# Optimization experiments

Hardware: AMD Instinct MI355X
Metric: run time of the kernel (lower is better)

Reference implementation:

```python
import jax, jax.numpy as jnp
import numpy as np

DIM = 192
HEADS = 6
WS = 8          # window size
SHIFT = 4       # shift size
HIDDEN = 384    # mlp hidden = 2.0 * dim
EPS = 1e-5


def _rel_pos_index(ws):
    # static [N, N] int index into the (2*ws-1)^2 bias table
    coords = np.stack(np.meshgrid(np.arange(ws), np.arange(ws), indexing='ij')).reshape(2, -1)
    rel = (coords[:, :, None] - coords[:, None, :]).transpose(1, 2, 0)
    rel[..., 0] += ws - 1
    rel[..., 1] += ws - 1
    rel[..., 0] *= 2 * ws - 1
    return rel.sum(-1)


def _attn_mask(hp, wp, ws, shift):
    # static shift-window mask: [nW, N, N], 0 or -100
    img = np.zeros((hp, wp))
    sl = (slice(0, -ws), slice(-ws, -shift), slice(-shift, None))
    cnt = 0
    for hs in sl:
        for wsl in sl:
            img[hs, wsl] = cnt
            cnt += 1
    m = img.reshape(hp // ws, ws, wp // ws, ws).transpose(0, 2, 1, 3).reshape(-1, ws * ws)
    diff = m[:, None, :] - m[:, :, None]
    return np.where(diff != 0, -100.0, 0.0).astype(np.float32)


def _ln(x, g, b):
    mu = x.mean(-1, keepdims=True)
    var = ((x - mu) ** 2).mean(-1, keepdims=True)
    return (x - mu) * jax.lax.rsqrt(var + EPS) * g + b


def setup_inputs() -> dict:
    key = jax.random.key(0)
    ks = jax.random.split(key, 6)
    B, H, W, C = 4, 224, 224, DIM
    return {
        'x': jax.random.normal(ks[0], (B, H * W, C), jnp.float32),
        'norm1_g': jnp.ones((C,), jnp.float32),
        'norm1_b': jnp.zeros((C,), jnp.float32),
        'qkv_w': jax.random.normal(ks[1], (C, 3 * C), jnp.float32) * 0.02,
        'qkv_b': jnp.zeros((3 * C,), jnp.float32),
        'proj_w': jax.random.normal(ks[2], (C, C), jnp.float32) * 0.02,
        'proj_b': jnp.zeros((C,), jnp.float32),
        'rel_bias_table': jax.random.normal(ks[3], ((2 * WS - 1) ** 2, HEADS), jnp.float32) * 0.02,
        'norm2_g': jnp.ones((C,), jnp.float32),
        'norm2_b': jnp.zeros((C,), jnp.float32),
        'fc1_w': jax.random.normal(ks[4], (C, HIDDEN), jnp.float32) * 0.02,
        'fc1_b': jnp.zeros((HIDDEN,), jnp.float32),
        'fc2_w': jax.random.normal(ks[5], (HIDDEN, C), jnp.float32) * 0.02,
        'fc2_b': jnp.zeros((C,), jnp.float32),
        'height': 224,
        'width': 224,
    }


def reference(x, norm1_g, norm1_b, qkv_w, qkv_b, proj_w, proj_b, rel_bias_table,
              norm2_g, norm2_b, fc1_w, fc1_b, fc2_w, fc2_b, height, width):
    B, T, C = x.shape
    dh = C // HEADS
    scale = dh ** (-0.5)
    shortcut = x

    xw = _ln(x, norm1_g, norm1_b).reshape(B, height, width, C)
    pad_h = (WS - height % WS) % WS
    pad_w = (WS - width % WS) % WS
    if pad_h > 0 or pad_w > 0:
        xw = jnp.pad(xw, ((0, 0), (0, pad_h), (0, pad_w), (0, 0)))
    Hp, Wp = height + pad_h, width + pad_w

    if SHIFT > 0:
        xs = jnp.roll(xw, (-SHIFT, -SHIFT), axis=(1, 2))
        mask = jnp.asarray(_attn_mask(Hp, Wp, WS, SHIFT))  # [nW, N, N]
    else:
        xs, mask = xw, None

    N = WS * WS
    # window partition -> [B*nW, N, C]
    xwin = xs.reshape(B, Hp // WS, WS, Wp // WS, WS, C).transpose(0, 1, 3, 2, 4, 5).reshape(-1, N, C)

    qkv = (xwin @ qkv_w + qkv_b).reshape(-1, N, 3, HEADS, dh).transpose(2, 0, 3, 1, 4)
    q, k, v = qkv[0] * scale, qkv[1], qkv[2]          # [B*nW, H, N, dh]
    attn = jnp.einsum('whnd,whmd->whnm', q, k)         # [B*nW, H, N, N]

    idx = jnp.asarray(_rel_pos_index(WS).reshape(-1))
    bias = rel_bias_table[idx].reshape(N, N, HEADS).transpose(2, 0, 1)  # [H, N, N]
    attn = attn + bias[None]

    if mask is not None:
        nW = mask.shape[0]
        attn = attn.reshape(-1, nW, HEADS, N, N) + mask[None, :, None]
        attn = attn.reshape(-1, HEADS, N, N)

    attn = jax.nn.softmax(attn, axis=-1)
    out = jnp.einsum('whnm,whmd->wnhd', attn, v).reshape(-1, N, C)
    out = out @ proj_w + proj_b

    # window reverse -> [B, Hp, Wp, C]
    out = out.reshape(B, Hp // WS, Wp // WS, WS, WS, C).transpose(0, 1, 3, 2, 4, 5).reshape(B, Hp, Wp, C)
    if SHIFT > 0:
        out = jnp.roll(out, (SHIFT, SHIFT), axis=(1, 2))
    if pad_h > 0 or pad_w > 0:
        out = out[:, :height, :width, :]

    x = shortcut + out.reshape(B, height * width, C)
    h = _ln(x, norm2_g, norm2_b)
    h = jax.nn.gelu(h @ fc1_w + fc1_b, approximate=False) @ fc2_w + fc2_b
    return x + h
```

## Files before the change

kernel.cpp:

```cpp
#include <hip/hip_runtime.h>
#include <math.h>

#define T_TOT   200704
#define C_DIM   192
#define HEADS   6
#define DH      32
#define NTOK    64
#define NWIN    3136
#define HID     384
#define IMG     224
#define NSIDE   28
#define WPI     784
#define QSCALE  0.17677669529663687f

typedef unsigned short ushortT;
typedef short bf16x8 __attribute__((ext_vector_type(8)));
typedef float f32x4 __attribute__((ext_vector_type(4)));

__device__ __forceinline__ float bf_lo(unsigned u){ return __uint_as_float(u << 16); }
__device__ __forceinline__ float bf_hi(unsigned u){ return __uint_as_float(u & 0xFFFF0000u); }
__device__ __forceinline__ unsigned short f2bf(float f){
    unsigned u = __float_as_uint(f);
    u += 0x7FFFu + ((u >> 16) & 1u);
    return (unsigned short)(u >> 16);
}
__device__ __forceinline__ unsigned pack2(float a, float b){
    return (unsigned)f2bf(a) | ((unsigned)f2bf(b) << 16);
}

__global__ void k_wprep(const float* __restrict__ w, unsigned short* __restrict__ o, int K, int N)
{
    int idx = blockIdx.x * 256 + threadIdx.x;
    if (idx >= K * N) return;
    int n = idx / K, k = idx - n * K;
    o[idx] = f2bf(w[(size_t)k * N + n]);
}

__global__ void k_bmprep(const float* __restrict__ table, float* __restrict__ bmT)
{
    int idx = blockIdx.x * 256 + threadIdx.x;
    int q = idx & 63, m = (idx >> 6) & 63;
    int head = (idx >> 12) % HEADS, type = idx / (64 * 64 * HEADS);
    int rq = q >> 3, cq = q & 7, rm = m >> 3, cm = m & 7;
    float b = table[((rq - rm + 7) * 15 + (cq - cm + 7)) * HEADS + head];
    int th = type >> 1, tw = type & 1;
    int lq = (th ? (rq >= 4 ? 2 : 1) : 0) * 3 + (tw ? (cq >= 4 ? 2 : 1) : 0);
    int lm = (th ? (rm >= 4 ? 2 : 1) : 0) * 3 + (tw ? (cm >= 4 ? 2 : 1) : 0);
    bmT[idx] = b + ((lq != lm) ? -100.f : 0.f);
}

__global__ void k_ln1qkv(const float* __restrict__ x, const float* __restrict__ g,
                         const float* __restrict__ bta,
                         const unsigned short* __restrict__ wt, const float* __restrict__ bias,
                         unsigned short* __restrict__ q, unsigned short* __restrict__ k,
                         unsigned short* __restrict__ v)
{
    __shared__ __align__(16) unsigned short As[64*200];
    const int tid = threadIdx.x, lane = tid & 63, wid = tid >> 6;
    const int lr = lane & 15, lg = lane >> 4;
    const int win = blockIdx.x;

    {
        int n = tid >> 2, part = tid & 3;
        int bimg = win / WPI, w2 = win % WPI;
        int wi = w2 / NSIDE, wj = w2 % NSIDE;
        int r = n >> 3, c = n & 7;
        int hs = wi * 8 + r + 4; if (hs >= IMG) hs -= IMG;
        int ws = wj * 8 + c + 4; if (ws >= IMG) ws -= IMG;
        size_t s = ((size_t)bimg * (IMG*IMG) + hs * IMG + ws) * C_DIM;
        const float* xp = x + s + part * 48;
        float vals[48];
        float sum = 0.f, sq = 0.f;
        #pragma unroll
        for (int j = 0; j < 12; j++){
            float4 v4 = *(const float4*)(xp + j*4);
            vals[j*4+0] = v4.x; vals[j*4+1] = v4.y; vals[j*4+2] = v4.z; vals[j*4+3] = v4.w;
            sum += v4.x + v4.y + v4.z + v4.w;
            sq  += v4.x*v4.x + v4.y*v4.y + v4.z*v4.z + v4.w*v4.w;
        }
        sum += __shfl_xor(sum, 1); sq += __shfl_xor(sq, 1);
        sum += __shfl_xor(sum, 2); sq += __shfl_xor(sq, 2);
        float mu = sum * (1.f/192.f);
        float var = sq * (1.f/192.f) - mu*mu;
        float rs = rsqrtf(var + 1e-5f);
        int c0 = part * 48;
        #pragma unroll
        for (int j = 0; j < 6; j++){
            int cc = c0 + j*8;
            float4 ga = *(const float4*)(g + cc), gb = *(const float4*)(g + cc + 4);
            float4 ba = *(const float4*)(bta + cc), bb = *(const float4*)(bta + cc + 4);
            unsigned short tmp[8];
            tmp[0] = f2bf((vals[j*8+0]-mu)*rs*ga.x + ba.x);
            tmp[1] = f2bf((vals[j*8+1]-mu)*rs*ga.y + ba.y);
            tmp[2] = f2bf((vals[j*8+2]-mu)*rs*ga.z + ba.z);
            tmp[3] = f2bf((vals[j*8+3]-mu)*rs*ga.w + ba.w);
            tmp[4] = f2bf((vals[j*8+4]-mu)*rs*gb.x + bb.x);
            tmp[5] = f2bf((vals[j*8+5]-mu)*rs*gb.y + bb.y);
            tmp[6] = f2bf((vals[j*8+6]-mu)*rs*gb.z + bb.z);
            tmp[7] = f2bf((vals[j*8+7]-mu)*rs*gb.w + bb.w);
            *(uint4*)&As[n*200 + cc] = *(uint4*)tmp;
        }
    }
    __syncthreads();

    #pragma unroll
    for (int chunk = 0; chunk < 3; chunk++){
        f32x4 acc[3][4];
        #pragma unroll
        for (int nf = 0; nf < 3; nf++)
            #pragma unroll
            for (int mf = 0; mf < 4; mf++)
                acc[nf][mf] = (f32x4){0.f,0.f,0.f,0.f};
        #pragma unroll
        for (int k0 = 0; k0 < C_DIM; k0 += 32){
            bf16x8 a[4], b[3];
            #pragma unroll
            for (int mf = 0; mf < 4; mf++)
                a[mf] = *(const bf16x8*)&As[(mf*16 + lr)*200 + k0 + lg*8];
            #pragma unroll
            for (int nf = 0; nf < 3; nf++)
                b[nf] = *(const bf16x8*)(wt + (size_t)(chunk*192 + wid*48 + nf*16 + lr)*C_DIM + k0 + lg*8);
            #pragma unroll
            for (int nf = 0; nf < 3; nf++)
                #pragma unroll
                for (int mf = 0; mf < 4; mf++)
                    acc[nf][mf] = __builtin_amdgcn_mfma_f32_16x16x32_bf16(a[mf], b[nf], acc[nf][mf], 0, 0, 0);
        }
        unsigned short* dst = (chunk == 0) ? q : (chunk == 1) ? k : v;
        float sc = (chunk == 0) ? QSCALE : 1.f;
        #pragma unroll
        for (int nf = 0; nf < 3; nf++){
            int cc = wid*48 + nf*16 + lr;
            float b = bias[chunk*192 + cc];
            int head = cc >> 5, d = cc & 31;
            unsigned short* dp = dst + ((size_t)(win*HEADS + head) * NTOK) * DH + d;
            #pragma unroll
            for (int mf = 0; mf < 4; mf++)
                #pragma unroll
                for (int r = 0; r < 4; r++){
                    int ntok = mf*16 + lg*4 + r;
                    dp[ntok*DH] = f2bf((acc[nf][mf][r] + b) * sc);
                }
        }
    }
}

__global__ void k_attn_mfma(const unsigned short* __restrict__ q, const unsigned short* __restrict__ k,
                            const unsigned short* __restrict__ v, const float* __restrict__ bmT,
                            unsigned short* __restrict__ attn_o)
{
    __shared__ __align__(16) unsigned short Vt[4][32*72];
    __shared__ __align__(16) unsigned short Ps[4][64*72];
    const int tid = threadIdx.x, lane = tid & 63, wid = tid >> 6;
    const int wh = blockIdx.x * 4 + wid;
    const int head = wh % HEADS, win = wh / HEADS;
    const int w2 = win % WPI;
    const int type = ((w2 / NSIDE) == 27 ? 2 : 0) + ((w2 % NSIDE) == 27 ? 1 : 0);
    const size_t base = (size_t)wh * (NTOK * DH);
    const int lr = lane & 15, lg = lane >> 4;

    {
        const uint4* vp = (const uint4*)(v + base + lane * DH);
        uint4 va = vp[0], vb = vp[1], vc = vp[2], vd = vp[3];
        unsigned short* dst = &Vt[wid][lane];
        unsigned w0[8] = {va.x, va.y, va.z, va.w, vb.x, vb.y, vb.z, vb.w};
        #pragma unroll
        for (int j = 0; j < 8; j++){
            dst[(2*j)*72]   = (unsigned short)(w0[j] & 0xFFFFu);
            dst[(2*j+1)*72] = (unsigned short)(w0[j] >> 16);
        }
        unsigned w1[8] = {vc.x, vc.y, vc.z, vc.w, vd.x, vd.y, vd.z, vd.w};
        #pragma unroll
        for (int j = 0; j < 8; j++){
            dst[(16+2*j)*72]   = (unsigned short)(w1[j] & 0xFFFFu);
            dst[(16+2*j+1)*72] = (unsigned short)(w1[j] >> 16);
        }
    }

    bf16x8 aq[4], bk[4];
    {
        const unsigned short* qg = q + base + lr * DH + (lg << 3);
        const unsigned short* kg = k + base + lr * DH + (lg << 3);
        #pragma unroll
        for (int i = 0; i < 4; i++){
            aq[i] = *(const bf16x8*)(qg + i * 16 * DH);
            bk[i] = *(const bf16x8*)(kg + i * 16 * DH);
        }
    }

    f32x4 acc[4][4];
    #pragma unroll
    for (int mi = 0; mi < 4; mi++)
        #pragma unroll
        for (int ni = 0; ni < 4; ni++)
            acc[mi][ni] = __builtin_amdgcn_mfma_f32_16x16x32_bf16(aq[mi], bk[ni],
                              (f32x4){0.f,0.f,0.f,0.f}, 0, 0, 0);

    const float* bmBase = bmT + ((size_t)(type * HEADS + head) * 64) * 64;
    #pragma unroll
    for (int mi = 0; mi < 4; mi++)
        #pragma unroll
        for (int ni = 0; ni < 4; ni++){
            float4 bm = *(const float4*)(bmBase + (lr + 16*ni)*64 + lg*4 + 16*mi);
            acc[mi][ni][0] += bm.x; acc[mi][ni][1] += bm.y;
            acc[mi][ni][2] += bm.z; acc[mi][ni][3] += bm.w;
        }

    #pragma unroll
    for (int mi = 0; mi < 4; mi++){
        #pragma unroll
        for (int r = 0; r < 4; r++){
            float mx = fmaxf(fmaxf(acc[mi][0][r], acc[mi][1][r]),
                             fmaxf(acc[mi][2][r], acc[mi][3][r]));
            mx = fmaxf(mx, __shfl_xor(mx, 1));
            mx = fmaxf(mx, __shfl_xor(mx, 2));
            mx = fmaxf(mx, __shfl_xor(mx, 4));
            mx = fmaxf(mx, __shfl_xor(mx, 8));
            float e0 = __expf(acc[mi][0][r] - mx);
            float e1 = __expf(acc[mi][1][r] - mx);
            float e2 = __expf(acc[mi][2][r] - mx);
            float e3 = __expf(acc[mi][3][r] - mx);
            float sum = e0 + e1 + e2 + e3;
            sum += __shfl_xor(sum, 1);
            sum += __shfl_xor(sum, 2);
            sum += __shfl_xor(sum, 4);
            sum += __shfl_xor(sum, 8);
            float inv = 1.f / sum;
            int row = lg*4 + r + 16*mi;
            unsigned short* pr = &Ps[wid][row*72 + lr];
            pr[0]  = f2bf(e0 * inv);
            pr[16] = f2bf(e1 * inv);
            pr[32] = f2bf(e2 * inv);
            pr[48] = f2bf(e3 * inv);
        }
    }

    f32x4 o[4][2];
    #pragma unroll
    for (int mi = 0; mi < 4; mi++)
        #pragma unroll
        for (int ni = 0; ni < 2; ni++)
            o[mi][ni] = (f32x4){0.f,0.f,0.f,0.f};
    #pragma unroll
    for (int kb = 0; kb < 2; kb++){
        bf16x8 ap[4], bv[2];
        #pragma unroll
        for (int mi = 0; mi < 4; mi++)
            ap[mi] = *(const bf16x8*)&Ps[wid][(lr + 16*mi)*72 + (lg<<3) + 32*kb];
        #pragma unroll
        for (int ni = 0; ni < 2; ni++)
            bv[ni] = *(const bf16x8*)&Vt[wid][(lr + 16*ni)*72 + (lg<<3) + 32*kb];
        #pragma unroll
        for (int mi = 0; mi < 4; mi++)
            #pragma unroll
            for (int ni = 0; ni < 2; ni++)
                o[mi][ni] = __builtin_amdgcn_mfma_f32_16x16x32_bf16(ap[mi], bv[ni], o[mi][ni], 0, 0, 0);
    }

    unsigned short* ob = attn_o + ((size_t)win * NTOK) * C_DIM + head * DH;
    #pragma unroll
    for (int mi = 0; mi < 4; mi++)
        #pragma unroll
        for (int ni = 0; ni < 2; ni++)
            #pragma unroll
            for (int r = 0; r < 4; r++){
                int row = lg*4 + r + 16*mi;
                ob[(size_t)row * C_DIM + lr + 16*ni] = f2bf(o[mi][ni][r]);
            }
}

template<int KTOT>
__device__ __forceinline__ void mfma_tile(const unsigned short* __restrict__ A,
                                          const unsigned short* __restrict__ Wt,
                                          int t0, int n0,
                                          f32x4 acc[4][2],
                                          unsigned short* As, unsigned short* Bs)
{
    const int tid = threadIdx.x;
    const int lane = tid & 63, wid = tid >> 6;
    const int wm = wid >> 1, wn = wid & 1;
    const int lr = lane & 15, lk = (lane >> 4) << 3;
    #pragma unroll
    for (int i = 0; i < 4; i++)
        #pragma unroll
        for (int j = 0; j < 2; j++)
            acc[i][j] = (f32x4){0.f, 0.f, 0.f, 0.f};

    const int arow = tid >> 1, asoff = (tid & 1) << 4;

    for (int k0 = 0; k0 < KTOT; k0 += 32){
        __syncthreads();
        {
            const unsigned short* ga = A + (size_t)(t0 + arow)*KTOT + k0 + asoff;
            *(uint4*)&As[arow*40 + asoff]     = *(const uint4*)(ga);
            *(uint4*)&As[arow*40 + asoff + 8] = *(const uint4*)(ga + 8);
            if (tid < 128){
                const unsigned short* gb = Wt + (size_t)(n0 + arow)*KTOT + k0 + asoff;
                *(uint4*)&Bs[arow*40 + asoff]     = *(const uint4*)(gb);
                *(uint4*)&Bs[arow*40 + asoff + 8] = *(const uint4*)(gb + 8);
            }
        }
        __syncthreads();
        bf16x8 b0 = *(const bf16x8*)&Bs[(wn*32 +      lr)*40 + lk];
        bf16x8 b1 = *(const bf16x8*)&Bs[(wn*32 + 16 + lr)*40 + lk];
        #pragma unroll
        for (int mf = 0; mf < 4; mf++){
            bf16x8 a = *(const bf16x8*)&As[(wm*64 + mf*16 + lr)*40 + lk];
            acc[mf][0] = __builtin_amdgcn_mfma_f32_16x16x32_bf16(a, b0, acc[mf][0], 0, 0, 0);
            acc[mf][1] = __builtin_amdgcn_mfma_f32_16x16x32_bf16(a, b1, acc[mf][1], 0, 0, 0);
        }
    }
}

__global__ void k_proj_m(const unsigned short* __restrict__ ain, const unsigned short* __restrict__ wt,
                         const float* __restrict__ bias, const float* __restrict__ x,
                         float* __restrict__ out)
{
    __shared__ __align__(16) unsigned short As[128*40];
    __shared__ __align__(16) unsigned short Bs[64*40];
    int t0 = blockIdx.x * 128, n0 = blockIdx.y * 64;
    f32x4 acc[4][2];
    mfma_tile<C_DIM>(ain, wt, t0, n0, acc, As, Bs);

    const int tid = threadIdx.x, lane = tid & 63, wid = tid >> 6;
    const int wm = wid >> 1, wn = wid & 1, lr = lane & 15;
    float b0 = bias[n0 + wn*32 + lr];
    float b1 = bias[n0 + wn*32 + 16 + lr];
    #pragma unroll
    for (int mf = 0; mf < 4; mf++){
        #pragma unroll
        for (int r = 0; r < 4; r++){
            int t = t0 + wm*64 + mf*16 + ((lane >> 4) << 2) + r;
            int win = t >> 6, n = t & 63;
            int bimg = win / WPI, w2 = win % WPI;
            int wi = w2 / NSIDE, wj = w2 % NSIDE;
            int rr = n >> 3, cc = n & 7;
            int hf = wi*8 + rr + 4; if (hf >= IMG) hf -= IMG;
            int wf = wj*8 + cc + 4; if (wf >= IMG) wf -= IMG;
            size_t s = ((size_t)bimg*(IMG*IMG) + hf*IMG + wf) * C_DIM;
            int c0 = n0 + wn*32 + lr;
            out[s + c0]      = x[s + c0]      + acc[mf][0][r] + b0;
            out[s + c0 + 16] = x[s + c0 + 16] + acc[mf][1][r] + b1;
        }
    }
}

#define XS_STR 200
#define H1_STR 392
#define O_STR  196
__global__ void k_mlp(float* __restrict__ out,
                      const float* __restrict__ g, const float* __restrict__ bta,
                      const unsigned short* __restrict__ w1, const float* __restrict__ b1,
                      const unsigned short* __restrict__ w2, const float* __restrict__ b2)
{
    __shared__ __align__(16) unsigned short H1u[32*H1_STR];
    unsigned short* Xs = H1u;
    float* O = (float*)H1u;
    const int tid = threadIdx.x, lane = tid & 63, wid = tid >> 6;
    const int lr = lane & 15, lg = lane >> 4;
    const int t0 = blockIdx.x * 32;

    {
        int row = tid >> 3, part = tid & 7;
        const float* xp = out + (size_t)(t0 + row) * C_DIM + part * 24;
        float vals[24];
        float sum = 0.f, sq = 0.f;
        #pragma unroll
        for (int j = 0; j < 6; j++){
            float4 v4 = *(const float4*)(xp + j*4);
            vals[j*4+0] = v4.x; vals[j*4+1] = v4.y; vals[j*4+2] = v4.z; vals[j*4+3] = v4.w;
            sum += v4.x + v4.y + v4.z + v4.w;
            sq  += v4.x*v4.x + v4.y*v4.y + v4.z*v4.z + v4.w*v4.w;
        }
        sum += __shfl_xor(sum, 1); sq += __shfl_xor(sq, 1);
        sum += __shfl_xor(sum, 2); sq += __shfl_xor(sq, 2);
        sum += __shfl_xor(sum, 4); sq += __shfl_xor(sq, 4);
        float mu = sum * (1.f/192.f);
        float var = sq * (1.f/192.f) - mu*mu;
        float rs = rsqrtf(var + 1e-5f);
        int c0 = part * 24;
        #pragma unroll
        for (int j = 0; j < 3; j++){
            int c = c0 + j*8;
            float4 ga = *(const float4*)(g + c), gb = *(const float4*)(g + c + 4);
            float4 ba = *(const float4*)(bta + c), bb = *(const float4*)(bta + c + 4);
            unsigned short tmp[8];
            tmp[0] = f2bf((vals[j*8+0]-mu)*rs*ga.x + ba.x);
            tmp[1] = f2bf((vals[j*8+1]-mu)*rs*ga.y + ba.y);
            tmp[2] = f2bf((vals[j*8+2]-mu)*rs*ga.z + ba.z);
            tmp[3] = f2bf((vals[j*8+3]-mu)*rs*ga.w + ba.w);
            tmp[4] = f2bf((vals[j*8+4]-mu)*rs*gb.x + bb.x);
            tmp[5] = f2bf((vals[j*8+5]-mu)*rs*gb.y + bb.y);
            tmp[6] = f2bf((vals[j*8+6]-mu)*rs*gb.z + bb.z);
            tmp[7] = f2bf((vals[j*8+7]-mu)*rs*gb.w + bb.w);
            *(uint4*)&Xs[row*XS_STR + c] = *(uint4*)tmp;
        }
    }
    __syncthreads();

    f32x4 acc1[6][2];
    {
        #pragma unroll
        for (int mf = 0; mf < 6; mf++)
            #pragma unroll
            for (int nf = 0; nf < 2; nf++)
                acc1[mf][nf] = (f32x4){0.f,0.f,0.f,0.f};
        #pragma unroll
        for (int k0 = 0; k0 < C_DIM; k0 += 32){
            bf16x8 a[6], b[2];
            #pragma unroll
            for (int mf = 0; mf < 6; mf++)
                a[mf] = *(const bf16x8*)(w1 + (size_t)(wid*96 + mf*16 + lr)*C_DIM + k0 + lg*8);
            #pragma unroll
            for (int nf = 0; nf < 2; nf++)
                b[nf] = *(const bf16x8*)&Xs[(nf*16 + lr)*XS_STR + k0 + lg*8];
            #pragma unroll
            for (int mf = 0; mf < 6; mf++)
                #pragma unroll
                for (int nf = 0; nf < 2; nf++)
                    acc1[mf][nf] = __builtin_amdgcn_mfma_f32_16x16x32_bf16(a[mf], b[nf], acc1[mf][nf], 0, 0, 0);
        }
    }
    __syncthreads();

    {
        #pragma unroll
        for (int mf = 0; mf < 6; mf++){
            int hc = wid*96 + mf*16 + lg*4;
            float4 bb = *(const float4*)(b1 + hc);
            float bias[4] = {bb.x, bb.y, bb.z, bb.w};
            #pragma unroll
            for (int nf = 0; nf < 2; nf++){
                int token = nf*16 + lr;
                float gl[4];
                #pragma unroll
                for (int r = 0; r < 4; r++){
                    float u = acc1[mf][nf][r] + bias[r];
                    gl[r] = 0.5f*u*(1.f + erff(u*0.70710678118654752f));
                }
                uint2 pk; pk.x = pack2(gl[0], gl[1]); pk.y = pack2(gl[2], gl[3]);
                *(uint2*)&H1u[token*H1_STR + hc] = pk;
            }
        }
    }
    __syncthreads();

    f32x4 acc2[2][3];
    {
        #pragma unroll
        for (int rf = 0; rf < 2; rf++)
            #pragma unroll
            for (int cf = 0; cf < 3; cf++)
                acc2[rf][cf] = (f32x4){0.f,0.f,0.f,0.f};
        #pragma unroll
        for (int k0 = 0; k0 < HID; k0 += 32){
            bf16x8 a[2], b[3];
            #pragma unroll
            for (int rf = 0; rf < 2; rf++)
                a[rf] = *(const bf16x8*)&H1u[(rf*16 + lr)*H1_STR + k0 + lg*8];
            #pragma unroll
            for (int cf = 0; cf < 3; cf++)
                b[cf] = *(const bf16x8*)(w2 + (size_t)(wid*48 + cf*16 + lr)*HID + k0 + lg*8);
            #pragma unroll
            for (int rf = 0; rf < 2; rf++)
                #pragma unroll
                for (int cf = 0; cf < 3; cf++)
                    acc2[rf][cf] = __builtin_amdgcn_mfma_f32_16x16x32_bf16(a[rf], b[cf], acc2[rf][cf], 0, 0, 0);
        }
    }
    __syncthreads();

    #pragma unroll
    for (int cf = 0; cf < 3; cf++){
        int c = wid*48 + cf*16 + lr;
        float bias = b2[c];
        #pragma unroll
        for (int rf = 0; rf < 2; rf++)
            #pragma unroll
            for (int r = 0; r < 4; r++)
                O[(rf*16 + lg*4 + r)*O_STR + c] = acc2[rf][cf][r] + bias;
    }
    __syncthreads();

    {
        int row = tid >> 3, part = tid & 7;
        float* op = out + (size_t)(t0 + row) * C_DIM;
        const float* Or = O + row * O_STR;
        #pragma unroll
        for (int j = 0; j < 6; j++){
            int c = part*4 + j*32;
            float4 add = *(const float4*)&Or[c];
            float4 old = *(const float4*)&op[c];
            old.x += add.x; old.y += add.y; old.z += add.z; old.w += add.w;
            *(float4*)&op[c] = old;
        }
    }
}

extern "C" void kernel_launch(void* const* d_in, const int* in_sizes, int n_in,
                              void* d_out, int out_size, void* d_ws, size_t ws_size,
                              hipStream_t stream)
{
    const float* x       = (const float*)d_in[0];
    const float* n1g     = (const float*)d_in[1];
    const float* n1b     = (const float*)d_in[2];
    const float* qkv_w   = (const float*)d_in[3];
    const float* qkv_b   = (const float*)d_in[4];
    const float* proj_w  = (const float*)d_in[5];
    const float* proj_b  = (const float*)d_in[6];
    const float* rtab    = (const float*)d_in[7];
    const float* n2g     = (const float*)d_in[8];
    const float* n2b     = (const float*)d_in[9];
    const float* fc1_w   = (const float*)d_in[10];
    const float* fc1_b   = (const float*)d_in[11];
    const float* fc2_w   = (const float*)d_in[12];
    const float* fc2_b   = (const float*)d_in[13];
    float* out = (float*)d_out;

    char* wsb = (char*)d_ws;
    const size_t SZ = (size_t)T_TOT * C_DIM * 2;
    unsigned short* attn_o = (unsigned short*)(wsb);
    unsigned short* qb   = (unsigned short*)(wsb + SZ);
    unsigned short* kb   = (unsigned short*)(wsb + 2*SZ);
    unsigned short* vb   = (unsigned short*)(wsb + 3*SZ);
    unsigned short* wt_qkv  = (unsigned short*)(wsb + 4*SZ);
    unsigned short* wt_proj = wt_qkv + 576*192;
    unsigned short* wt_fc1  = wt_proj + 192*192;
    unsigned short* wt_fc2  = wt_fc1 + 384*192;
    float*          bmT     = (float*)(wt_fc2 + 384*192);

    k_wprep<<<(192*576 + 255)/256, 256, 0, stream>>>(qkv_w, wt_qkv, 192, 576);
    k_wprep<<<(192*192 + 255)/256, 256, 0, stream>>>(proj_w, wt_proj, 192, 192);
    k_wprep<<<(192*384 + 255)/256, 256, 0, stream>>>(fc1_w, wt_fc1, 192, 384);
    k_wprep<<<(384*192 + 255)/256, 256, 0, stream>>>(fc2_w, wt_fc2, 384, 192);
    k_bmprep<<<(4*HEADS*64*64)/256, 256, 0, stream>>>(rtab, bmT);

    k_ln1qkv<<<NWIN, 256, 0, stream>>>(x, n1g, n1b, wt_qkv, qkv_b, qb, kb, vb);
    k_attn_mfma<<<NWIN*HEADS/4, 256, 0, stream>>>(qb, kb, vb, bmT, attn_o);
    k_proj_m<<<dim3(T_TOT/128, 3), 256, 0, stream>>>(attn_o, wt_proj, proj_b, x, out);
    k_mlp<<<T_TOT/32, 256, 0, stream>>>(out, n2g, n2b, wt_fc1, fc1_b, wt_fc2, fc2_b);
}
```

Measured before the change: 760.7 us.

## Split LN1 into its own kernel and rewrite projection as per-window MFMA

LayerNorm1 plus the window gather now run in a separate kernel that writes a bf16 windowed buffer, and the QKV GEMM reads that buffer directly. The projection GEMM is rewritten as one block per window with the full 192-wide output, reading weights straight from global memory. This drops the per-k-step LDS staging and barriers and computes window coordinates once per block. The cost is an extra kernel launch and a bf16 round trip of the normalized activations through global memory.

Result: faster. 685.0 us (-9.9%).

```diff
diff --git a/kernel.cpp b/kernel.cpp
--- a/kernel.cpp
+++ b/kernel.cpp
@@ -17,8 +17,6 @@
 typedef short bf16x8 __attribute__((ext_vector_type(8)));
 typedef float f32x4 __attribute__((ext_vector_type(4)));
 
-__device__ __forceinline__ float bf_lo(unsigned u){ return __uint_as_float(u << 16); }
-__device__ __forceinline__ float bf_hi(unsigned u){ return __uint_as_float(u & 0xFFFF0000u); }
 __device__ __forceinline__ unsigned short f2bf(float f){
     unsigned u = __float_as_uint(f);
     u += 0x7FFFu + ((u >> 16) & 1u);
@@ -49,56 +47,51 @@
     bmT[idx] = b + ((lq != lm) ? -100.f : 0.f);
 }
 
-__global__ void k_ln1qkv(const float* __restrict__ x, const float* __restrict__ g,
-                         const float* __restrict__ bta,
-                         const unsigned short* __restrict__ wt, const float* __restrict__ bias,
-                         unsigned short* __restrict__ q, unsigned short* __restrict__ k,
-                         unsigned short* __restrict__ v)
+__global__ void k_ln1_win(const float* __restrict__ x, const float* __restrict__ g,
+                          const float* __restrict__ bta, unsigned short* __restrict__ xwin)
+{
+    int t    = blockIdx.x * 4 + (threadIdx.x >> 6);
+    int lane = threadIdx.x & 63;
+    int win = t >> 6, n = t & 63;
+    int bimg = win / WPI, w2 = win % WPI;
+    int wi = w2 / NSIDE, wj = w2 % NSIDE;
+    int r = n >> 3, c = n & 7;
+    int hs = wi * 8 + r + 4; if (hs >= IMG) hs -= IMG;
+    int ws = wj * 8 + c + 4; if (ws >= IMG) ws -= IMG;
+    int s = bimg * (IMG*IMG) + hs * IMG + ws;
+    const float* xp = x + (size_t)s * C_DIM + lane * 3;
+    float v0 = xp[0], v1 = xp[1], v2 = xp[2];
+    float sum = v0 + v1 + v2;
+    float sq  = v0*v0 + v1*v1 + v2*v2;
+    #pragma unroll
+    for (int m = 1; m < 64; m <<= 1){ sum += __shfl_xor(sum, m); sq += __shfl_xor(sq, m); }
+    float mu = sum * (1.f/192.f);
+    float var = sq * (1.f/192.f) - mu*mu;
+    float rs = rsqrtf(var + 1e-5f);
+    int j = lane * 3;
+    unsigned short* op = xwin + (size_t)t * C_DIM + j;
+    op[0] = f2bf((v0-mu)*rs*g[j]   + bta[j]);
+    op[1] = f2bf((v1-mu)*rs*g[j+1] + bta[j+1]);
+    op[2] = f2bf((v2-mu)*rs*g[j+2] + bta[j+2]);
+}
+
+__global__ void k_qkv_m(const unsigned short* __restrict__ xwin, const unsigned short* __restrict__ wt,
+                        const float* __restrict__ bias,
+                        unsigned short* __restrict__ q, unsigned short* __restrict__ k,
+                        unsigned short* __restrict__ v)
 {
     __shared__ __align__(16) unsigned short As[64*200];
     const int tid = threadIdx.x, lane = tid & 63, wid = tid >> 6;
     const int lr = lane & 15, lg = lane >> 4;
-    const int win = blockIdx.x;
-
-    {
-        int n = tid >> 2, part = tid & 3;
-        int bimg = win / WPI, w2 = win % WPI;
-        int wi = w2 / NSIDE, wj = w2 % NSIDE;
-        int r = n >> 3, c = n & 7;
-        int hs = wi * 8 + r + 4; if (hs >= IMG) hs -= IMG;
-        int ws = wj * 8 + c + 4; if (ws >= IMG) ws -= IMG;
-        size_t s = ((size_t)bimg * (IMG*IMG) + hs * IMG + ws) * C_DIM;
-        const float* xp = x + s + part * 48;
-        float vals[48];
-        float sum = 0.f, sq = 0.f;
-        #pragma unroll
-        for (int j = 0; j < 12; j++){
-            float4 v4 = *(const float4*)(xp + j*4);
-            vals[j*4+0] = v4.x; vals[j*4+1] = v4.y; vals[j*4+2] = v4.z; vals[j*4+3] = v4.w;
-            sum += v4.x + v4.y + v4.z + v4.w;
-            sq  += v4.x*v4.x + v4.y*v4.y + v4.z*v4.z + v4.w*v4.w;
-        }
-        sum += __shfl_xor(sum, 1); sq += __shfl_xor(sq, 1);
-        sum += __shfl_xor(sum, 2); sq += __shfl_xor(sq, 2);
-        float mu = sum * (1.f/192.f);
-        float var = sq * (1.f/192.f) - mu*mu;
-        float rs = rsqrtf(var + 1e-5f);
-        int c0 = part * 48;
+    const int t0 = blockIdx.x * 64, win = blockIdx.x;
+
+    {
+        int row = tid >> 2, part = tid & 3;
+        const unsigned short* gp = xwin + (size_t)(t0 + row) * C_DIM;
         #pragma unroll
         for (int j = 0; j < 6; j++){
-            int cc = c0 + j*8;
-            float4 ga = *(const float4*)(g + cc), gb = *(const float4*)(g + cc + 4);
-            float4 ba = *(const float4*)(bta + cc), bb = *(const float4*)(bta + cc + 4);
-            unsigned short tmp[8];
-            tmp[0] = f2bf((vals[j*8+0]-mu)*rs*ga.x + ba.x);
-            tmp[1] = f2bf((vals[j*8+1]-mu)*rs*ga.y + ba.y);
-            tmp[2] = f2bf((vals[j*8+2]-mu)*rs*ga.z + ba.z);
-            tmp[3] = f2bf((vals[j*8+3]-mu)*rs*ga.w + ba.w);
-            tmp[4] = f2bf((vals[j*8+4]-mu)*rs*gb.x + bb.x);
-            tmp[5] = f2bf((vals[j*8+5]-mu)*rs*gb.y + bb.y);
-            tmp[6] = f2bf((vals[j*8+6]-mu)*rs*gb.z + bb.z);
-            tmp[7] = f2bf((vals[j*8+7]-mu)*rs*gb.w + bb.w);
-            *(uint4*)&As[n*200 + cc] = *(uint4*)tmp;
+            int c = part*8 + j*32;
+            *(uint4*)&As[row*200 + c] = *(const uint4*)(gp + c);
         }
     }
     __syncthreads();
@@ -269,78 +262,64 @@
             }
 }
 
-template<int KTOT>
-__device__ __forceinline__ void mfma_tile(const unsigned short* __restrict__ A,
-                                          const unsigned short* __restrict__ Wt,
-                                          int t0, int n0,
-                                          f32x4 acc[4][2],
-                                          unsigned short* As, unsigned short* Bs)
-{
-    const int tid = threadIdx.x;
-    const int lane = tid & 63, wid = tid >> 6;
-    const int wm = wid >> 1, wn = wid & 1;
-    const int lr = lane & 15, lk = (lane >> 4) << 3;
-    #pragma unroll
-    for (int i = 0; i < 4; i++)
-        #pragma unroll
-        for (int j = 0; j < 2; j++)
-            acc[i][j] = (f32x4){0.f, 0.f, 0.f, 0.f};
-
-    const int arow = tid >> 1, asoff = (tid & 1) << 4;
-
-    for (int k0 = 0; k0 < KTOT; k0 += 32){
-        __syncthreads();
-        {
-            const unsigned short* ga = A + (size_t)(t0 + arow)*KTOT + k0 + asoff;
-            *(uint4*)&As[arow*40 + asoff]     = *(const uint4*)(ga);
-            *(uint4*)&As[arow*40 + asoff + 8] = *(const uint4*)(ga + 8);
-            if (tid < 128){
-                const unsigned short* gb = Wt + (size_t)(n0 + arow)*KTOT + k0 + asoff;
-                *(uint4*)&Bs[arow*40 + asoff]     = *(const uint4*)(gb);
-                *(uint4*)&Bs[arow*40 + asoff + 8] = *(const uint4*)(gb + 8);
+__global__ void k_proj2(const unsigned short* __restrict__ ain, const unsigned short* __restrict__ wt,
+                        const float* __restrict__ bias, const float* __restrict__ x,
+                        float* __restrict__ out)
+{
+    __shared__ __align__(16) unsigned short As[64*200];
+    const int tid = threadIdx.x, lane = tid & 63, wid = tid >> 6;
+    const int lr = lane & 15, lg = lane >> 4;
+    const int t0 = blockIdx.x * 64, win = blockIdx.x;
+
+    {
+        int row = tid >> 2, part = tid & 3;
+        const unsigned short* gp = ain + (size_t)(t0 + row) * C_DIM;
+        #pragma unroll
+        for (int j = 0; j < 6; j++){
+            int c = part*8 + j*32;
+            *(uint4*)&As[row*200 + c] = *(const uint4*)(gp + c);
+        }
+    }
+    __syncthreads();
+
+    f32x4 acc[3][4];
+    #pragma unroll
+    for (int nf = 0; nf < 3; nf++)
+        #pragma unroll
+        for (int mf = 0; mf < 4; mf++)
+            acc[nf][mf] = (f32x4){0.f,0.f,0.f,0.f};
+    #pragma unroll
+    for (int k0 = 0; k0 < C_DIM; k0 += 32){
+        bf16x8 a[4], b[3];
+        #pragma unroll
+        for (int mf = 0; mf < 4; mf++)
+            a[mf] = *(const bf16x8*)&As[(mf*16 + lr)*200 + k0 + lg*8];
+        #pragma unroll
+        for (int nf = 0; nf < 3; nf++)
+            b[nf] = *(const bf16x8*)(wt + (size_t)(wid*48 + nf*16 + lr)*C_DIM + k0 + lg*8);
+        #pragma unroll
+        for (int nf = 0; nf < 3; nf++)
+            #pragma unroll
+            for (int mf = 0; mf < 4; mf++)
+                acc[nf][mf] = __builtin_amdgcn_mfma_f32_16x16x32_bf16(a[mf], b[nf], acc[nf][mf], 0, 0, 0);
+    }
+
+    const int bimg = win / WPI, w2 = win % WPI;
+    const int wi = w2 / NSIDE, wj = w2 % NSIDE;
+    #pragma unroll
+    for (int mf = 0; mf < 4; mf++){
+        #pragma unroll
+        for (int r = 0; r < 4; r++){
+            int n = mf*16 + lg*4 + r;
+            int rr = n >> 3, cc_ = n & 7;
+            int hf = wi*8 + rr + 4; if (hf >= IMG) hf -= IMG;
+            int wf = wj*8 + cc_ + 4; if (wf >= IMG) wf -= IMG;
+            size_t s = ((size_t)bimg*(IMG*IMG) + hf*IMG + wf) * C_DIM;
+            #pragma unroll
+            for (int nf = 0; nf < 3; nf++){
+                int c = wid*48 + nf*16 + lr;
+                out[s + c] = x[s + c] + acc[nf][mf][r] + bias[c];
             }
-        }
-        __syncthreads();
-        bf16x8 b0 = *(const bf16x8*)&Bs[(wn*32 +      lr)*40 + lk];
-        bf16x8 b1 = *(const bf16x8*)&Bs[(wn*32 + 16 + lr)*40 + lk];
-        #pragma unroll
-        for (int mf = 0; mf < 4; mf++){
-            bf16x8 a = *(const bf16x8*)&As[(wm*64 + mf*16 + lr)*40 + lk];
-            acc[mf][0] = __builtin_amdgcn_mfma_f32_16x16x32_bf16(a, b0, acc[mf][0], 0, 0, 0);
-            acc[mf][1] = __builtin_amdgcn_mfma_f32_16x16x32_bf16(a, b1, acc[mf][1], 0, 0, 0);
-        }
-    }
-}
-
-__global__ void k_proj_m(const unsigned short* __restrict__ ain, const unsigned short* __restrict__ wt,
-                         const float* __restrict__ bias, const float* __restrict__ x,
-                         float* __restrict__ out)
-{
-    __shared__ __align__(16) unsigned short As[128*40];
-    __shared__ __align__(16) unsigned short Bs[64*40];
-    int t0 = blockIdx.x * 128, n0 = blockIdx.y * 64;
-    f32x4 acc[4][2];
-    mfma_tile<C_DIM>(ain, wt, t0, n0, acc, As, Bs);
-
-    const int tid = threadIdx.x, lane = tid & 63, wid = tid >> 6;
-    const int wm = wid >> 1, wn = wid & 1, lr = lane & 15;
-    float b0 = bias[n0 + wn*32 + lr];
-    float b1 = bias[n0 + wn*32 + 16 + lr];
-    #pragma unroll
-    for (int mf = 0; mf < 4; mf++){
-        #pragma unroll
-        for (int r = 0; r < 4; r++){
-            int t = t0 + wm*64 + mf*16 + ((lane >> 4) << 2) + r;
-            int win = t >> 6, n = t & 63;
-            int bimg = win / WPI, w2 = win % WPI;
-            int wi = w2 / NSIDE, wj = w2 % NSIDE;
-            int rr = n >> 3, cc = n & 7;
-            int hf = wi*8 + rr + 4; if (hf >= IMG) hf -= IMG;
-            int wf = wj*8 + cc + 4; if (wf >= IMG) wf -= IMG;
-            size_t s = ((size_t)bimg*(IMG*IMG) + hf*IMG + wf) * C_DIM;
-            int c0 = n0 + wn*32 + lr;
-            out[s + c0]      = x[s + c0]      + acc[mf][0][r] + b0;
-            out[s + c0 + 16] = x[s + c0 + 16] + acc[mf][1][r] + b1;
         }
     }
 }
@@ -519,7 +498,7 @@
 
     char* wsb = (char*)d_ws;
     const size_t SZ = (size_t)T_TOT * C_DIM * 2;
-    unsigned short* attn_o = (unsigned short*)(wsb);
+    unsigned short* xwin = (unsigned short*)(wsb);
     unsigned short* qb   = (unsigned short*)(wsb + SZ);
     unsigned short* kb   = (unsigned short*)(wsb + 2*SZ);
     unsigned short* vb   = (unsigned short*)(wsb + 3*SZ);
@@ -528,6 +507,7 @@
     unsigned short* wt_fc1  = wt_proj + 192*192;
     unsigned short* wt_fc2  = wt_fc1 + 384*192;
     float*          bmT     = (float*)(wt_fc2 + 384*192);
+    unsigned short* attn_o = xwin;
 
     k_wprep<<<(192*576 + 255)/256, 256, 0, stream>>>(qkv_w, wt_qkv, 192, 576);
     k_wprep<<<(192*192 + 255)/256, 256, 0, stream>>>(proj_w, wt_proj, 192, 192);
@@ -535,8 +515,9 @@
     k_wprep<<<(384*192 + 255)/256, 256, 0, stream>>>(fc2_w, wt_fc2, 384, 192);
     k_bmprep<<<(4*HEADS*64*64)/256, 256, 0, stream>>>(rtab, bmT);
 
-    k_ln1qkv<<<NWIN, 256, 0, stream>>>(x, n1g, n1b, wt_qkv, qkv_b, qb, kb, vb);
+    k_ln1_win<<<T_TOT/4, 256, 0, stream>>>(x, n1g, n1b, xwin);
+    k_qkv_m<<<NWIN, 256, 0, stream>>>(xwin, wt_qkv, qkv_b, qb, kb, vb);
     k_attn_mfma<<<NWIN*HEADS/4, 256, 0, stream>>>(qb, kb, vb, bmT, attn_o);
-    k_proj_m<<<dim3(T_TOT/128, 3), 256, 0, stream>>>(attn_o, wt_proj, proj_b, x, out);
+    k_proj2<<<NWIN, 256, 0, stream>>>(attn_o, wt_proj, proj_b, x, out);
     k_mlp<<<T_TOT/32, 256, 0, stream>>>(out, n2g, n2b, wt_fc1, fc1_b, wt_fc2, fc2_b);
 }
```
